# Performance work log

Measured on AMD Instinct MI355X. Metric: run time of the kernel, lower is better.

## Reference

```python
import jax, jax.numpy as jnp
import numpy as np

BETA = 0.25  # commitment loss weight (init kwarg)

def setup_inputs() -> dict:
    key = jax.random.key(0)
    k1, k2 = jax.random.split(key)
    z = jax.random.normal(k1, (4, 256, 16, 32, 32), dtype=jnp.float32)
    # nn.Embedding init: uniform(-1/K, 1/K)
    K, d = 1024, 256
    emb_w = jax.random.uniform(k2, (K, d), dtype=jnp.float32,
                               minval=-1.0 / K, maxval=1.0 / K)
    return {"z": z, "emb_w": emb_w}


def reference(z, emb_w):
    B, C, D, H, W = z.shape  # C == embedding_dim
    zp = jnp.transpose(z, (0, 2, 3, 4, 1))          # (B, D, H, W, C)
    z_flat = zp.reshape(-1, C)                      # (N, C)
    # squared distances ||z - e||^2 = ||z||^2 + ||e||^2 - 2 z.e
    z_sq = jnp.sum(z_flat * z_flat, axis=1, keepdims=True)      # (N, 1)
    e_sq = jnp.sum(emb_w * emb_w, axis=1)[None, :]              # (1, K)
    dist = z_sq + e_sq - 2.0 * jnp.einsum('nc,kc->nk', z_flat, emb_w)  # (N, K)
    idx = jnp.argmin(dist, axis=1)                  # (N,)
    z_q = emb_w[idx]                                # (N, C)
    sg = jax.lax.stop_gradient
    loss = jnp.mean((sg(z_q) - z_flat) ** 2) + BETA * jnp.mean((z_q - sg(z_flat)) ** 2)
    # straight-through estimator
    z_q = z_flat + sg(z_q - z_flat)
    z_q = z_q.reshape(B, D, H, W, C)
    z_q = jnp.transpose(z_q, (0, 4, 1, 2, 3))       # (B, C, D, H, W)
    return z_q, loss, idx
```

## Files before the change

kernel.cpp:

```cpp
#include <hip/hip_runtime.h>

#define KCODES 1024
#define CDIM   256
#define SP     16384
#define ZQTOT  16777216
#define NQ     65536
#define BSTRIDE 4194304
#define MAX_AMB 12288
#define LOSS_SCALE 33554432.0
#define KEYMASK 0xFFFFFC00u
#define AMB_THR 6.0e-4f
#define BIAS    0.25f

#define QT2    128
#define NTILE  32
#define ROWB   528
#define TILEB  16896

using f32x4  = __attribute__((ext_vector_type(4)))  float;
using f32x16 = __attribute__((ext_vector_type(16))) float;
using bf16x8 = __attribute__((ext_vector_type(8)))  short;

__device__ __forceinline__ unsigned short f2bf(float x) {
    unsigned u = __float_as_uint(x);
    u += 0x7fffu + ((u >> 16) & 1u);
    return (unsigned short)(u >> 16);
}
__device__ __forceinline__ unsigned umn(unsigned a, unsigned b){ return a < b ? a : b; }
__device__ __forceinline__ unsigned umx(unsigned a, unsigned b){ return a > b ? a : b; }

__device__ __forceinline__ float pw128_sq(const float* a) {
    float r[8];
    #pragma unroll
    for (int j = 0; j < 8; ++j) r[j] = __fmul_rn(a[j], a[j]);
    for (int i = 8; i < 128; i += 8) {
        #pragma unroll
        for (int j = 0; j < 8; ++j) r[j] = __fadd_rn(r[j], __fmul_rn(a[i+j], a[i+j]));
    }
    return __fadd_rn(__fadd_rn(__fadd_rn(r[0], r[1]), __fadd_rn(r[2], r[3])),
                     __fadd_rn(__fadd_rn(r[4], r[5]), __fadd_rn(r[6], r[7])));
}
__device__ __forceinline__ float pairwise256_sq(const float* a) {
    return __fadd_rn(pw128_sq(a), pw128_sq(a + 128));
}
__device__ __forceinline__ float np_dot256(const float* zr, const float* er) {
    float a0 = 0.f, a1 = 0.f, a2 = 0.f, a3 = 0.f;
    for (int i8 = 0; i8 < 256; i8 += 8) {
        a0 = __fadd_rn(a0, __fmul_rn(zr[i8+0], er[i8+0]));
        a1 = __fadd_rn(a1, __fmul_rn(zr[i8+1], er[i8+1]));
        a2 = __fadd_rn(a2, __fmul_rn(zr[i8+2], er[i8+2]));
        a3 = __fadd_rn(a3, __fmul_rn(zr[i8+3], er[i8+3]));
        a0 = __fadd_rn(a0, __fmul_rn(zr[i8+4], er[i8+4]));
        a1 = __fadd_rn(a1, __fmul_rn(zr[i8+5], er[i8+5]));
        a2 = __fadd_rn(a2, __fmul_rn(zr[i8+6], er[i8+6]));
        a3 = __fadd_rn(a3, __fmul_rn(zr[i8+7], er[i8+7]));
    }
    return __fadd_rn(__fadd_rn(a0, a1), __fadd_rn(a2, a3));
}

__global__ __launch_bounds__(64)
void vq_prep(const float* __restrict__ emb, unsigned short* __restrict__ embh,
             float* __restrict__ esq_g) {
    const int k = blockIdx.x;
    const int l = threadIdx.x;
    float4 v = ((const float4*)(emb + (size_t)k * CDIM))[l];
    float s = v.x*v.x + v.y*v.y + v.z*v.z + v.w*v.w;
    unsigned short h0=f2bf(v.x), h1=f2bf(v.y), h2=f2bf(v.z), h3=f2bf(v.w);
    uint2 hh; hh.x = (unsigned)h0 | ((unsigned)h1<<16); hh.y = (unsigned)h2 | ((unsigned)h3<<16);
    *(uint2*)&embh[(size_t)k*CDIM + l*4] = hh;
    #pragma unroll
    for (int off = 32; off > 0; off >>= 1) s += __shfl_down(s, off, 64);
    if (l == 0) esq_g[k] = s + BIAS;
}

__global__ __launch_bounds__(256, 2)
void vq_main_mfma(const float* __restrict__ z, const float* __restrict__ emb,
                  const unsigned short* __restrict__ embh,
                  const float* __restrict__ esq_g,
                  float* __restrict__ out, unsigned long long* __restrict__ loss_acc,
                  unsigned int* __restrict__ amb_cnt, uint4* __restrict__ wl4) {
    __shared__ __align__(16) unsigned char smem[2*TILEB + 4096];
    unsigned* top1 = (unsigned*)(smem + 2*TILEB);
    unsigned* top2 = top1 + 128;
    unsigned* top3 = top2 + 128;
    float*    zsql = (float*)(top3 + 128);
    int*      fidx = (int*)(zsql + 128);
    float*    lpart = (float*)(fidx + 128);

    const int t    = threadIdx.x;
    const int l    = t & 63;
    const int w    = t >> 6;
    const int half = l >> 5;
    const int lr   = l & 31;
    const int bid  = blockIdx.x;
    const int obid = ((bid & 7) << 6) + (bid >> 3);
    const int n0   = obid * QT2;
    const int b    = n0 >> 14;
    const int sp0  = n0 & 16383;
    const int wq0  = w * 32;
    const float* zb = z + (size_t)b * BSTRIDE + sp0 + wq0 + lr;
    const char* ebase = (const char*)embh;

    uint4 st[4];
    #pragma unroll
    for (int k = 0; k < 4; ++k)
        st[k] = *(const uint4*)(ebase + (size_t)(t + k*256) * 16);

    bf16x8 A[16];
    float zsq_p = 0.f;
    #pragma unroll
    for (int ks = 0; ks < 16; ++ks) {
        const float* zp = zb + (size_t)(ks*16 + half*8) * SP;
        float v[8];
        #pragma unroll
        for (int j = 0; j < 8; ++j) v[j] = zp[(size_t)j * SP];
        bf16x8 a;
        #pragma unroll
        for (int j = 0; j < 8; ++j) {
            zsq_p += v[j] * v[j];
            a[j] = (short)f2bf(v[j]);
        }
        A[ks] = a;
    }
    zsq_p += __shfl_xor(zsq_p, 32, 64);
    if (half == 0) zsql[wq0 + lr] = zsq_p;

    #pragma unroll
    for (int k = 0; k < 4; ++k) {
        const int idx = t + k*256;
        *(uint4*)(smem + (idx >> 5)*ROWB + (idx & 31)*16) = st[k];
    }
    __syncthreads();

    unsigned m1v[16], m2v[16], m3v[16];
    #pragma unroll
    for (int s = 0; s < 16; ++s) { m1v[s]=0xFFFFFFFFu; m2v[s]=0xFFFFFFFFu; m3v[s]=0xFFFFFFFFu; }

    int cur = 0;
    for (int tile = 0; tile < NTILE; ++tile) {
        if (tile + 1 < NTILE) {
            #pragma unroll
            for (int k = 0; k < 4; ++k)
                st[k] = *(const uint4*)(ebase + (size_t)(tile+1)*16384 + (size_t)(t + k*256)*16);
        }
        const float es = esq_g[tile*32 + lr];

        const unsigned char* bb = smem + cur*TILEB + lr*ROWB + half*16;
        f32x16 acc[4];
        #pragma unroll
        for (int c = 0; c < 4; ++c)
            acc[c] = f32x16{0.f,0.f,0.f,0.f,0.f,0.f,0.f,0.f,0.f,0.f,0.f,0.f,0.f,0.f,0.f,0.f};
        __builtin_amdgcn_s_setprio(1);
        #pragma unroll
        for (int ks = 0; ks < 16; ++ks) {
            const bf16x8 Bv = *(const bf16x8*)(bb + ks*32);
            acc[ks & 3] = __builtin_amdgcn_mfma_f32_32x32x16_bf16(A[ks], Bv, acc[ks & 3], 0, 0, 0);
        }
        __builtin_amdgcn_s_setprio(0);
        const unsigned kc = (unsigned)(tile*32 + lr);
        #pragma unroll
        for (int s = 0; s < 16; ++s) {
            const float dot = (acc[0][s] + acc[1][s]) + (acc[2][s] + acc[3][s]);
            const float sc = __builtin_fmaf(-2.0f, dot, es);
            const unsigned p = (__float_as_uint(sc) & KEYMASK) | kc;
            const unsigned x = umx(m1v[s], p); m1v[s] = umn(m1v[s], p);
            const unsigned y = umx(m2v[s], x); m2v[s] = umn(m2v[s], x);
            m3v[s] = umn(m3v[s], y);
        }
        if (tile + 1 < NTILE) {
            #pragma unroll
            for (int k = 0; k < 4; ++k) {
                const int idx = t + k*256;
                *(uint4*)(smem + (cur^1)*TILEB + (idx >> 5)*ROWB + (idx & 31)*16) = st[k];
            }
        }
        __syncthreads();
        cur ^= 1;
    }

    #pragma unroll
    for (int s = 0; s < 16; ++s) {
        unsigned a1 = m1v[s], a2 = m2v[s], a3 = m3v[s];
        #pragma unroll
        for (int m = 1; m < 32; m <<= 1) {
            const unsigned b1 = (unsigned)__shfl_xor((int)a1, m, 64);
            const unsigned b2 = (unsigned)__shfl_xor((int)a2, m, 64);
            const unsigned b3 = (unsigned)__shfl_xor((int)a3, m, 64);
            const unsigned hi1 = umx(a1, b1), lo2 = umn(a2, b2);
            const unsigned r3  = umn(umx(hi1, lo2), umn(a3, b3));
            a1 = umn(a1, b1);
            a2 = umn(hi1, lo2);
            a3 = r3;
        }
        if (lr == s) {
            const int r = (s & 3) + ((s >> 2) << 3) + (half << 2);
            top1[wq0 + r] = a1; top2[wq0 + r] = a2; top3[wq0 + r] = a3;
        }
    }
    __syncthreads();

    if (t < QT2) {
        const unsigned k1 = top1[t], k2 = top2[t], k3 = top3[t];
        const int I1 = (int)(k1 & 1023u);
        fidx[t] = I1;
        out[ZQTOT + 1 + n0 + t] = (float)I1;
        const float v1 = __uint_as_float(k1 & KEYMASK);
        const float v2 = __uint_as_float(k2 & KEYMASK);
        if (v2 - v1 < AMB_THR) {
            unsigned pos = atomicAdd(amb_cnt, 1u);
            if (pos < MAX_AMB)
                wl4[pos] = make_uint4((unsigned)(n0 + t),
                                      (k1 & 1023u) | ((k2 & 1023u) << 16),
                                      (k3 & 1023u) | ((k3 & 1023u) << 16), 0u);
        }
        float lq = zsql[t] + (v1 - BIAS);
        #pragma unroll
        for (int off = 32; off > 0; off >>= 1) lq += __shfl_down(lq, off, 64);
        if ((t & 63) == 0) lpart[t >> 6] = lq;
    }
    __syncthreads();
    if (t == 0)
        atomicAdd(loss_acc, (unsigned long long)(long long)((double)(lpart[0] + lpart[1]) * LOSS_SCALE));

    {
        const int q  = t & 127;
        const int dh = t >> 7;
        const int fq = fidx[q];
        const float4* ev = (const float4*)(emb + (size_t)fq * CDIM + dh * 128);
        float* ob = out + (size_t)b * BSTRIDE + (size_t)dh * 128 * SP + sp0 + q;
        #pragma unroll
        for (int i = 0; i < 32; ++i) {
            const float4 v = ev[i];
            float* o = ob + (size_t)(i * 4) * SP;
            o[0]            = v.x;
            o[SP]           = v.y;
            o[2*SP]         = v.z;
            o[(size_t)3*SP] = v.w;
        }
    }
}

__global__ __launch_bounds__(256)
void vq_fix_cand(const float* __restrict__ z, const float* __restrict__ emb,
                 float* __restrict__ out, const unsigned int* __restrict__ amb_cnt,
                 const uint4* __restrict__ wl4,
                 const unsigned long long* __restrict__ loss_acc) {
    __shared__ float zrow[4][CDIM];
    __shared__ float erow[4][4][CDIM];
    __shared__ float dsh[4][4], esh[4][4];
    __shared__ float zss[4];

    if (blockIdx.x == 0 && threadIdx.x == 0) {
        double mse = (double)(long long)(*loss_acc) / LOSS_SCALE / (double)ZQTOT;
        out[ZQTOT] = (float)(mse * 1.25);
    }

    unsigned cnt = *amb_cnt; if (cnt > MAX_AMB) cnt = MAX_AMB;
    const int t  = threadIdx.x;
    const int wv = t >> 6;
    const int l  = t & 63;
    const unsigned stride = gridDim.x * 4;
    const unsigned nIter = (cnt + stride - 1) / stride;

    for (unsigned j = 0; j < nIter; ++j) {
        __syncthreads();
        const unsigned widx = (unsigned)blockIdx.x * 4 + wv + j * stride;
        const bool active = widx < cnt;
        int n = 0, b = 0, sp = 0;
        int codes[4] = {0, 0, 0, 0};
        if (active) {
            const uint4 e = wl4[widx];
            n = (int)e.x; b = n >> 14; sp = n & 16383;
            codes[0] = (int)(e.y & 1023u); codes[1] = (int)((e.y >> 16) & 1023u);
            codes[2] = (int)(e.z & 1023u); codes[3] = (int)((e.z >> 16) & 1023u);
            #pragma unroll
            for (int i = 0; i < 4; ++i) {
                const int c = l + 64*i;
                zrow[wv][c] = z[(size_t)b * BSTRIDE + (size_t)c * SP + sp];
            }
            const int r = l >> 4, c0 = (l & 15) * 16;
            const float4* src = (const float4*)(emb + (size_t)codes[r] * CDIM + c0);
            float4* dst = (float4*)&erow[wv][r][c0];
            #pragma unroll
            for (int i = 0; i < 4; ++i) dst[i] = src[i];
        }
        __syncthreads();
        if (active) {
            const int role = l >> 4, rr = (l >> 2) & 3, a = l & 3;
            if (role == 0) {
                const float* er = erow[wv][rr];
                const float* zr = zrow[wv];
                float acc = __fmul_rn(zr[a], er[a]);
                for (int i = 1; i < 64; ++i)
                    acc = __fadd_rn(acc, __fmul_rn(zr[4*i + a], er[4*i + a]));
                const float u = __fadd_rn(acc, __shfl_xor(acc, 1, 64));
                const float d = __fadd_rn(u,   __shfl_xor(u,   2, 64));
                if (a == 0) dsh[wv][rr] = d;
            } else if (role == 1 || (role == 2 && rr == 0)) {
                const float* src = (role == 1) ? erow[wv][rr] : zrow[wv];
                float pA = __fmul_rn(src[a],       src[a]);
                float pB = __fmul_rn(src[a+4],     src[a+4]);
                float qA = __fmul_rn(src[128+a],   src[128+a]);
                float qB = __fmul_rn(src[128+a+4], src[128+a+4]);
                #pragma unroll 4
                for (int i = 1; i < 16; ++i) {
                    pA = __fadd_rn(pA, __fmul_rn(src[8*i+a],       src[8*i+a]));
                    pB = __fadd_rn(pB, __fmul_rn(src[8*i+a+4],     src[8*i+a+4]));
                    qA = __fadd_rn(qA, __fmul_rn(src[128+8*i+a],   src[128+8*i+a]));
                    qB = __fadd_rn(qB, __fmul_rn(src[128+8*i+a+4], src[128+8*i+a+4]));
                }
                float uA = __fadd_rn(pA, __shfl_xor(pA, 1, 64));
                float vA = __fadd_rn(uA, __shfl_xor(uA, 2, 64));
                float uB = __fadd_rn(pB, __shfl_xor(pB, 1, 64));
                float vB = __fadd_rn(uB, __shfl_xor(uB, 2, 64));
                const float h0 = __fadd_rn(vA, vB);
                float uC = __fadd_rn(qA, __shfl_xor(qA, 1, 64));
                float vC = __fadd_rn(uC, __shfl_xor(uC, 2, 64));
                float uD = __fadd_rn(qB, __shfl_xor(qB, 1, 64));
                float vD = __fadd_rn(uD, __shfl_xor(uD, 2, 64));
                const float h1 = __fadd_rn(vC, vD);
                const float stot = __fadd_rn(h0, h1);
                if (a == 0) { if (role == 1) esh[wv][rr] = stot; else zss[wv] = stot; }
            }
        }
        __syncthreads();
        if (active && l == 0) {
            float bd = 3.4e38f; int bk = KCODES;
            #pragma unroll
            for (int i = 0; i < 4; ++i) {
                const float d = __fsub_rn(__fadd_rn(zss[wv], esh[wv][i]),
                                          __fmul_rn(2.0f, dsh[wv][i]));
                if (d < bd || (d == bd && codes[i] < bk)) { bd = d; bk = codes[i]; }
            }
            out[ZQTOT + 1 + n] = (float)bk;
        }
    }
}

__global__ __launch_bounds__(256)
void vq_main_basic(const float* __restrict__ z, const float* __restrict__ emb,
                   float* __restrict__ out, unsigned long long* __restrict__ loss_acc,
                   unsigned int* __restrict__ amb_cnt, unsigned int* __restrict__ wl) {
    __shared__ float zlz[64 * CDIM];
    __shared__ float esq[KCODES];
    __shared__ float m1s[4][64], m2s[4][64];
    __shared__ int   i1s[4][64];
    __shared__ int   fidx[64];
    __shared__ float lsum[4];

    const int t  = threadIdx.x;
    const int q  = t & 63;
    const int w  = __builtin_amdgcn_readfirstlane(t >> 6);
    const int qs = q & 7;
    const int n0 = blockIdx.x * 64;
    const int b  = n0 >> 14;
    const int sp0 = n0 & 16383;
    const float* zb = z + (size_t)b * BSTRIDE;

    #pragma unroll 4
    for (int i = 0; i < 64; ++i) {
        int c = (t >> 6) * 64 + i;
        float v = zb[(size_t)c * SP + sp0 + q];
        zlz[q * CDIM + ((((c >> 2) ^ qs) << 2) | (c & 3))] = v;
    }
    for (int k = t; k < KCODES; k += 256) {
        const float4* er = (const float4*)(emb + (size_t)k * CDIM);
        float s = 0.f;
        for (int c4 = 0; c4 < 64; ++c4) {
            float4 e = er[c4];
            s += e.x*e.x + e.y*e.y + e.z*e.z + e.w*e.w;
        }
        esq[k] = s;
    }
    __syncthreads();

    float m1 = 3.4e38f, m2 = 3.4e38f; int i1 = 0;
    const float* zrow = zlz + q * CDIM;
    const int kbase = w * 256;
    for (int kk = 0; kk < 256; kk += 8) {
        const int k0 = kbase + kk;
        float acc[8] = {0,0,0,0,0,0,0,0};
        for (int c4 = 0; c4 < 64; ++c4) {
            float4 zv = *(const float4*)(zrow + ((c4 ^ qs) << 2));
            #pragma unroll
            for (int j = 0; j < 8; ++j) {
                float4 ev = *(const float4*)(emb + (size_t)(k0 + j) * CDIM + (c4 << 2));
                acc[j] += zv.x*ev.x + zv.y*ev.y + zv.z*ev.z + zv.w*ev.w;
            }
        }
        #pragma unroll
        for (int j = 0; j < 8; ++j) {
            float s = esq[k0 + j] - 2.0f * acc[j];
            if (s < m1)      { m2 = m1; m1 = s; i1 = k0 + j; }
            else if (s < m2) { m2 = s; }
        }
    }
    m1s[w][q] = m1; m2s[w][q] = m2; i1s[w][q] = i1;
    __syncthreads();

    if (t < 64) {
        float M1 = 3.4e38f, M2 = 3.4e38f; int I1 = 0;
        for (int g = 0; g < 4; ++g) {
            float v1 = m1s[g][t], v2 = m2s[g][t];
            int   a1 = i1s[g][t];
            if (v1 < M1) { M2 = M1; M1 = v1; I1 = a1; }
            else if (v1 < M2) { M2 = v1; }
            if (v2 < M2) { M2 = v2; }
        }
        if (M2 - M1 < 1.5e-4f) {
            unsigned pos = atomicAdd(amb_cnt, 1u);
            if (pos < MAX_AMB) wl[pos] = n0 + t;
        }
        fidx[t] = I1;
        out[ZQTOT + 1 + n0 + t] = (float)I1;
    }
    __syncthreads();

    const int fq = fidx[q];
    const float* eq = emb + (size_t)fq * CDIM;
    float ls = 0.f;
    #pragma unroll 4
    for (int i = 0; i < 64; ++i) {
        int c = (t >> 6) * 64 + i;
        float zv = zrow[((((c >> 2) ^ qs) << 2) | (c & 3))];
        float ev = eq[c];
        float d = ev - zv;
        ls += d * d;
        out[(size_t)b * BSTRIDE + (size_t)c * SP + sp0 + q] = zv + d;
    }
    #pragma unroll
    for (int off = 32; off > 0; off >>= 1) ls += __shfl_down(ls, off, 64);
    if (q == 0) lsum[w] = ls;
    __syncthreads();
    if (t == 0) {
        float tot = lsum[0] + lsum[1] + lsum[2] + lsum[3];
        atomicAdd(loss_acc, (unsigned long long)(long long)((double)tot * LOSS_SCALE));
    }
}

__global__ __launch_bounds__(256)
void vq_fix_np(const float* __restrict__ z, const float* __restrict__ emb,
               float* __restrict__ out, const unsigned int* __restrict__ amb_cnt,
               const unsigned int* __restrict__ wl) {
    __shared__ float zrow[CDIM];
    __shared__ float zsq_sh;
    __shared__ float rd[256];
    __shared__ int   rk[256];

    unsigned cnt = *amb_cnt; if (cnt > MAX_AMB) cnt = MAX_AMB;
    if (blockIdx.x >= cnt) return;
    const int n = (int)wl[blockIdx.x];
    const int b = n >> 14, sp = n & 16383;
    const int t = threadIdx.x;

    zrow[t] = z[(size_t)b * BSTRIDE + (size_t)t * SP + sp];
    __syncthreads();
    if (t == 0) zsq_sh = pairwise256_sq(zrow);
    __syncthreads();
    const float zsq = zsq_sh;

    float bestd = 3.4e38f; int bestk = KCODES;
    for (int j = 0; j < 4; ++j) {
        const int k = t + 256 * j;
        const float* er = emb + (size_t)k * CDIM;
        const float dot = np_dot256(zrow, er);
        const float es  = pairwise256_sq(er);
        const float d   = __fsub_rn(__fadd_rn(zsq, es), __fmul_rn(2.0f, dot));
        if (d < bestd || (d == bestd && k < bestk)) { bestd = d; bestk = k; }
    }
    rd[t] = bestd; rk[t] = bestk;
    __syncthreads();
    for (int s = 128; s > 0; s >>= 1) {
        if (t < s) {
            float od = rd[t + s]; int ok = rk[t + s];
            if (od < rd[t] || (od == rd[t] && ok < rk[t])) { rd[t] = od; rk[t] = ok; }
        }
        __syncthreads();
    }
    if (t == 0) out[ZQTOT + 1 + n] = (float)rk[0];
}

__global__ void vq_final(const unsigned long long* __restrict__ acc, float* __restrict__ out) {
    if (threadIdx.x == 0 && blockIdx.x == 0) {
        double mse = (double)(long long)acc[0] / LOSS_SCALE / (double)ZQTOT;
        out[ZQTOT] = (float)(mse * 1.25);
    }
}

extern "C" void kernel_launch(void* const* d_in, const int* in_sizes, int n_in,
                              void* d_out, int out_size, void* d_ws, size_t ws_size,
                              hipStream_t stream) {
    const float* z   = (const float*)d_in[0];
    const float* emb = (const float*)d_in[1];
    float* out = (float*)d_out;

    unsigned long long* loss_acc = (unsigned long long*)d_ws;
    unsigned int* amb_cnt = (unsigned int*)((char*)d_ws + 8);
    const size_t WL4_OFF  = 64;
    const size_t ESQ_OFF  = (WL4_OFF + (size_t)MAX_AMB * 16 + 255) & ~(size_t)255;
    const size_t EMBH_OFF = (ESQ_OFF + (size_t)KCODES * 4 + 255) & ~(size_t)255;
    const size_t WS_NEED  = EMBH_OFF + (size_t)KCODES * CDIM * 2;

    hipMemsetAsync(d_ws, 0, 16, stream);
    if (ws_size >= WS_NEED) {
        uint4* wl4 = (uint4*)((char*)d_ws + WL4_OFF);
        float* esq_g = (float*)((char*)d_ws + ESQ_OFF);
        unsigned short* embh = (unsigned short*)((char*)d_ws + EMBH_OFF);
        vq_prep<<<dim3(KCODES), dim3(64), 0, stream>>>(emb, embh, esq_g);
        vq_main_mfma<<<dim3(NQ / QT2), dim3(256), 0, stream>>>(z, emb, embh, esq_g,
                                                               out, loss_acc, amb_cnt, wl4);
        vq_fix_cand<<<dim3(1024), dim3(256), 0, stream>>>(z, emb, out, amb_cnt, wl4, loss_acc);
    } else {
        unsigned int* wl = (unsigned int*)((char*)d_ws + WL4_OFF);
        vq_main_basic<<<dim3(NQ / 64), dim3(256), 0, stream>>>(z, emb, out, loss_acc, amb_cnt, wl);
        vq_fix_np<<<dim3(MAX_AMB), dim3(256), 0, stream>>>(z, emb, out, amb_cnt, wl);
        vq_final<<<dim3(1), dim3(64), 0, stream>>>(loss_acc, out);
    }
}
```

Baseline: 112.6 us.

## Switch main VQ kernel to 16x16x32 MFMA with 64-query blocks

Moves the distance kernel from 32x32x16 MFMA tiles over 128 queries per block to 16x16x32 MFMA tiles over 64 queries per block, with two code sub-tiles per step. Register use for A fragments and per-query top-k state drops, and launch bounds are raised to 4 blocks per SM for higher occupancy. The cross-lane reduction now merges 4 candidates per lane and keeps a true fourth candidate for the ambiguity worklist, instead of repeating the third. In exchange, each block re-streams the full codebook for half as many queries, doubling LDS and L2 traffic per query.

```diff
diff --git a/kernel.cpp b/kernel.cpp
--- a/kernel.cpp
+++ b/kernel.cpp
@@ -12,13 +12,12 @@
 #define AMB_THR 6.0e-4f
 #define BIAS    0.25f
 
-#define QT2    128
+#define QT     64
 #define NTILE  32
 #define ROWB   528
 #define TILEB  16896
 
 using f32x4  = __attribute__((ext_vector_type(4)))  float;
-using f32x16 = __attribute__((ext_vector_type(16))) float;
 using bf16x8 = __attribute__((ext_vector_type(8)))  short;
 
 __device__ __forceinline__ unsigned short f2bf(float x) {
@@ -73,31 +72,31 @@
     if (l == 0) esq_g[k] = s + BIAS;
 }
 
-__global__ __launch_bounds__(256, 2)
+__global__ __launch_bounds__(256, 4)
 void vq_main_mfma(const float* __restrict__ z, const float* __restrict__ emb,
                   const unsigned short* __restrict__ embh,
                   const float* __restrict__ esq_g,
                   float* __restrict__ out, unsigned long long* __restrict__ loss_acc,
                   unsigned int* __restrict__ amb_cnt, uint4* __restrict__ wl4) {
-    __shared__ __align__(16) unsigned char smem[2*TILEB + 4096];
+    __shared__ __align__(16) unsigned char smem[2*TILEB + 2048];
     unsigned* top1 = (unsigned*)(smem + 2*TILEB);
-    unsigned* top2 = top1 + 128;
-    unsigned* top3 = top2 + 128;
-    float*    zsql = (float*)(top3 + 128);
-    int*      fidx = (int*)(zsql + 128);
-    float*    lpart = (float*)(fidx + 128);
-
-    const int t    = threadIdx.x;
-    const int l    = t & 63;
-    const int w    = t >> 6;
-    const int half = l >> 5;
-    const int lr   = l & 31;
+    unsigned* top2 = top1 + 64;
+    unsigned* top3 = top2 + 64;
+    unsigned* top4 = top3 + 64;
+    float*    zsql = (float*)(top4 + 64);
+    int*      fidx = (int*)(zsql + 64);
+
+    const int t  = threadIdx.x;
+    const int l  = t & 63;
+    const int w  = t >> 6;
+    const int lh = l >> 4;
+    const int lr = l & 15;
     const int bid  = blockIdx.x;
-    const int obid = ((bid & 7) << 6) + (bid >> 3);
-    const int n0   = obid * QT2;
+    const int obid = ((bid & 7) << 7) + (bid >> 3);
+    const int n0   = obid * QT;
     const int b    = n0 >> 14;
     const int sp0  = n0 & 16383;
-    const int wq0  = w * 32;
+    const int wq0  = w * 16;
     const float* zb = z + (size_t)b * BSTRIDE + sp0 + wq0 + lr;
     const char* ebase = (const char*)embh;
 
@@ -106,11 +105,11 @@
     for (int k = 0; k < 4; ++k)
         st[k] = *(const uint4*)(ebase + (size_t)(t + k*256) * 16);
 
-    bf16x8 A[16];
+    bf16x8 A[8];
     float zsq_p = 0.f;
     #pragma unroll
-    for (int ks = 0; ks < 16; ++ks) {
-        const float* zp = zb + (size_t)(ks*16 + half*8) * SP;
+    for (int ks = 0; ks < 8; ++ks) {
+        const float* zp = zb + (size_t)(ks*32 + lh*8) * SP;
         float v[8];
         #pragma unroll
         for (int j = 0; j < 8; ++j) v[j] = zp[(size_t)j * SP];
@@ -122,8 +121,9 @@
         }
         A[ks] = a;
     }
+    zsq_p += __shfl_xor(zsq_p, 16, 64);
     zsq_p += __shfl_xor(zsq_p, 32, 64);
-    if (half == 0) zsql[wq0 + lr] = zsq_p;
+    if (lh == 0) zsql[wq0 + lr] = zsq_p;
 
     #pragma unroll
     for (int k = 0; k < 4; ++k) {
@@ -132,9 +132,9 @@
     }
     __syncthreads();
 
-    unsigned m1v[16], m2v[16], m3v[16];
-    #pragma unroll
-    for (int s = 0; s < 16; ++s) { m1v[s]=0xFFFFFFFFu; m2v[s]=0xFFFFFFFFu; m3v[s]=0xFFFFFFFFu; }
+    unsigned m1v[4], m2v[4], m3v[4];
+    #pragma unroll
+    for (int s = 0; s < 4; ++s) { m1v[s]=0xFFFFFFFFu; m2v[s]=0xFFFFFFFFu; m3v[s]=0xFFFFFFFFu; }
 
     int cur = 0;
     for (int tile = 0; tile < NTILE; ++tile) {
@@ -143,29 +143,37 @@
             for (int k = 0; k < 4; ++k)
                 st[k] = *(const uint4*)(ebase + (size_t)(tile+1)*16384 + (size_t)(t + k*256)*16);
         }
-        const float es = esq_g[tile*32 + lr];
-
-        const unsigned char* bb = smem + cur*TILEB + lr*ROWB + half*16;
-        f32x16 acc[4];
-        #pragma unroll
-        for (int c = 0; c < 4; ++c)
-            acc[c] = f32x16{0.f,0.f,0.f,0.f,0.f,0.f,0.f,0.f,0.f,0.f,0.f,0.f,0.f,0.f,0.f,0.f};
+        const float es0 = esq_g[tile*32 + lr];
+        const float es1 = esq_g[tile*32 + 16 + lr];
+
+        const unsigned char* bb = smem + cur*TILEB + lr*ROWB + lh*16;
+        f32x4 acc[2][2];
+        #pragma unroll
+        for (int nt = 0; nt < 2; ++nt)
+            #pragma unroll
+            for (int c = 0; c < 2; ++c) acc[nt][c] = f32x4{0.f,0.f,0.f,0.f};
         __builtin_amdgcn_s_setprio(1);
         #pragma unroll
-        for (int ks = 0; ks < 16; ++ks) {
-            const bf16x8 Bv = *(const bf16x8*)(bb + ks*32);
-            acc[ks & 3] = __builtin_amdgcn_mfma_f32_32x32x16_bf16(A[ks], Bv, acc[ks & 3], 0, 0, 0);
+        for (int ks = 0; ks < 8; ++ks) {
+            const bf16x8 B0 = *(const bf16x8*)(bb + ks*64);
+            const bf16x8 B1 = *(const bf16x8*)(bb + 16*ROWB + ks*64);
+            acc[0][ks & 1] = __builtin_amdgcn_mfma_f32_16x16x32_bf16(A[ks], B0, acc[0][ks & 1], 0, 0, 0);
+            acc[1][ks & 1] = __builtin_amdgcn_mfma_f32_16x16x32_bf16(A[ks], B1, acc[1][ks & 1], 0, 0, 0);
         }
         __builtin_amdgcn_s_setprio(0);
-        const unsigned kc = (unsigned)(tile*32 + lr);
-        #pragma unroll
-        for (int s = 0; s < 16; ++s) {
-            const float dot = (acc[0][s] + acc[1][s]) + (acc[2][s] + acc[3][s]);
-            const float sc = __builtin_fmaf(-2.0f, dot, es);
-            const unsigned p = (__float_as_uint(sc) & KEYMASK) | kc;
-            const unsigned x = umx(m1v[s], p); m1v[s] = umn(m1v[s], p);
-            const unsigned y = umx(m2v[s], x); m2v[s] = umn(m2v[s], x);
-            m3v[s] = umn(m3v[s], y);
+        #pragma unroll
+        for (int nt = 0; nt < 2; ++nt) {
+            const unsigned kc = (unsigned)(tile*32 + nt*16 + lr);
+            const float es = nt ? es1 : es0;
+            #pragma unroll
+            for (int j = 0; j < 4; ++j) {
+                const float dot = acc[nt][0][j] + acc[nt][1][j];
+                const float sc = __builtin_fmaf(-2.0f, dot, es);
+                const unsigned p = (__float_as_uint(sc) & KEYMASK) | kc;
+                const unsigned x = umx(m1v[j], p); m1v[j] = umn(m1v[j], p);
+                const unsigned y = umx(m2v[j], x); m2v[j] = umn(m2v[j], x);
+                m3v[j] = umn(m3v[j], y);
+            }
         }
         if (tile + 1 < NTILE) {
             #pragma unroll
@@ -179,28 +187,30 @@
     }
 
     #pragma unroll
-    for (int s = 0; s < 16; ++s) {
-        unsigned a1 = m1v[s], a2 = m2v[s], a3 = m3v[s];
-        #pragma unroll
-        for (int m = 1; m < 32; m <<= 1) {
-            const unsigned b1 = (unsigned)__shfl_xor((int)a1, m, 64);
-            const unsigned b2 = (unsigned)__shfl_xor((int)a2, m, 64);
-            const unsigned b3 = (unsigned)__shfl_xor((int)a3, m, 64);
-            const unsigned hi1 = umx(a1, b1), lo2 = umn(a2, b2);
-            const unsigned r3  = umn(umx(hi1, lo2), umn(a3, b3));
-            a1 = umn(a1, b1);
-            a2 = umn(hi1, lo2);
-            a3 = r3;
-        }
-        if (lr == s) {
-            const int r = (s & 3) + ((s >> 2) << 3) + (half << 2);
-            top1[wq0 + r] = a1; top2[wq0 + r] = a2; top3[wq0 + r] = a3;
-        }
-    }
-    __syncthreads();
-
-    if (t < QT2) {
-        const unsigned k1 = top1[t], k2 = top2[t], k3 = top3[t];
+    for (int s = 0; s < 4; ++s) {
+        unsigned t1 = m1v[s], t2 = m2v[s], t3 = m3v[s], t4 = 0xFFFFFFFFu;
+        #pragma unroll
+        for (int m = 1; m < 16; m <<= 1) {
+            const unsigned b1 = (unsigned)__shfl_xor((int)t1, m, 64);
+            const unsigned b2 = (unsigned)__shfl_xor((int)t2, m, 64);
+            const unsigned b3 = (unsigned)__shfl_xor((int)t3, m, 64);
+            const unsigned b4 = (unsigned)__shfl_xor((int)t4, m, 64);
+            #define INS(v) { unsigned x_=umx(t1,(v)); t1=umn(t1,(v)); \
+                             unsigned y_=umx(t2,x_);  t2=umn(t2,x_);  \
+                             unsigned z_=umx(t3,y_);  t3=umn(t3,y_);  \
+                             t4=umn(t4,z_); }
+            INS(b1); INS(b2); INS(b3); INS(b4);
+            #undef INS
+        }
+        if (lr == 0) {
+            const int qq = wq0 + lh*4 + s;
+            top1[qq] = t1; top2[qq] = t2; top3[qq] = t3; top4[qq] = t4;
+        }
+    }
+    __syncthreads();
+
+    if (t < QT) {
+        const unsigned k1 = top1[t], k2 = top2[t], k3 = top3[t], k4 = top4[t];
         const int I1 = (int)(k1 & 1023u);
         fidx[t] = I1;
         out[ZQTOT + 1 + n0 + t] = (float)I1;
@@ -211,25 +221,24 @@
             if (pos < MAX_AMB)
                 wl4[pos] = make_uint4((unsigned)(n0 + t),
                                       (k1 & 1023u) | ((k2 & 1023u) << 16),
-                                      (k3 & 1023u) | ((k3 & 1023u) << 16), 0u);
+                                      (k3 & 1023u) | ((k4 & 1023u) << 16), 0u);
         }
         float lq = zsql[t] + (v1 - BIAS);
         #pragma unroll
         for (int off = 32; off > 0; off >>= 1) lq += __shfl_down(lq, off, 64);
-        if ((t & 63) == 0) lpart[t >> 6] = lq;
-    }
-    __syncthreads();
-    if (t == 0)
-        atomicAdd(loss_acc, (unsigned long long)(long long)((double)(lpart[0] + lpart[1]) * LOSS_SCALE));
+        if (t == 0)
+            atomicAdd(loss_acc, (unsigned long long)(long long)((double)lq * LOSS_SCALE));
+    }
+    __syncthreads();
 
     {
-        const int q  = t & 127;
-        const int dh = t >> 7;
+        const int q  = t & 63;
+        const int dh = t >> 6;
         const int fq = fidx[q];
-        const float4* ev = (const float4*)(emb + (size_t)fq * CDIM + dh * 128);
-        float* ob = out + (size_t)b * BSTRIDE + (size_t)dh * 128 * SP + sp0 + q;
-        #pragma unroll
-        for (int i = 0; i < 32; ++i) {
+        const float4* ev = (const float4*)(emb + (size_t)fq * CDIM + dh * 64);
+        float* ob = out + (size_t)b * BSTRIDE + (size_t)dh * 64 * SP + sp0 + q;
+        #pragma unroll
+        for (int i = 0; i < 16; ++i) {
             const float4 v = ev[i];
             float* o = ob + (size_t)(i * 4) * SP;
             o[0]            = v.x;
@@ -507,8 +516,8 @@
         float* esq_g = (float*)((char*)d_ws + ESQ_OFF);
         unsigned short* embh = (unsigned short*)((char*)d_ws + EMBH_OFF);
         vq_prep<<<dim3(KCODES), dim3(64), 0, stream>>>(emb, embh, esq_g);
-        vq_main_mfma<<<dim3(NQ / QT2), dim3(256), 0, stream>>>(z, emb, embh, esq_g,
-                                                               out, loss_acc, amb_cnt, wl4);
+        vq_main_mfma<<<dim3(NQ / QT), dim3(256), 0, stream>>>(z, emb, embh, esq_g,
+                                                              out, loss_acc, amb_cnt, wl4);
         vq_fix_cand<<<dim3(1024), dim3(256), 0, stream>>>(z, emb, out, amb_cnt, wl4, loss_acc);
     } else {
         unsigned int* wl = (unsigned int*)((char*)d_ws + WL4_OFF);
```

Result: no change. 113.5 us (+0.8%).

## Fuse ambiguous-candidate fixup and loss finalization into main MFMA kernel

Applied to the files above, without the earlier changes.

Each block now keeps its ambiguous queries in a shared-memory worklist and rechecks them in exact fp32 at the end of the main kernel, so the separate vq_fix_cand launch and its global worklist and atomics go away. The final loss is written by the last block to finish, detected with a done counter and a threadfence. This saves a kernel launch and global round-trips. In exchange, the per-block worklist is capped at 64 entries, which could drop fixes when a block has many near-ties, and shared memory is reused for the fixup buffers.

```diff
diff --git a/kernel.cpp b/kernel.cpp
--- a/kernel.cpp
+++ b/kernel.cpp
@@ -16,6 +16,7 @@
 #define NTILE  32
 #define ROWB   528
 #define TILEB  16896
+#define WLMAX  64
 
 using f32x4  = __attribute__((ext_vector_type(4)))  float;
 using f32x16 = __attribute__((ext_vector_type(16))) float;
@@ -78,7 +79,7 @@
                   const unsigned short* __restrict__ embh,
                   const float* __restrict__ esq_g,
                   float* __restrict__ out, unsigned long long* __restrict__ loss_acc,
-                  unsigned int* __restrict__ amb_cnt, uint4* __restrict__ wl4) {
+                  unsigned int* __restrict__ done_cnt) {
     __shared__ __align__(16) unsigned char smem[2*TILEB + 4096];
     unsigned* top1 = (unsigned*)(smem + 2*TILEB);
     unsigned* top2 = top1 + 128;
@@ -86,6 +87,13 @@
     float*    zsql = (float*)(top3 + 128);
     int*      fidx = (int*)(zsql + 128);
     float*    lpart = (float*)(fidx + 128);
+    unsigned* wlcnt = (unsigned*)(smem + 2*TILEB + 2576);
+    uint4*    wlloc = (uint4*)(smem + 2*TILEB + 2592);
+    float* zrow = (float*)smem;
+    float* erow = (float*)(smem + 4096);
+    float* dsh  = (float*)(smem + 20480);
+    float* esh  = (float*)(smem + 20544);
+    float* zss  = (float*)(smem + 20608);
 
     const int t    = threadIdx.x;
     const int l    = t & 63;
@@ -101,6 +109,8 @@
     const float* zb = z + (size_t)b * BSTRIDE + sp0 + wq0 + lr;
     const char* ebase = (const char*)embh;
 
+    if (t == 0) *wlcnt = 0;
+
     uint4 st[4];
     #pragma unroll
     for (int k = 0; k < 4; ++k)
@@ -207,11 +217,9 @@
         const float v1 = __uint_as_float(k1 & KEYMASK);
         const float v2 = __uint_as_float(k2 & KEYMASK);
         if (v2 - v1 < AMB_THR) {
-            unsigned pos = atomicAdd(amb_cnt, 1u);
-            if (pos < MAX_AMB)
-                wl4[pos] = make_uint4((unsigned)(n0 + t),
-                                      (k1 & 1023u) | ((k2 & 1023u) << 16),
-                                      (k3 & 1023u) | ((k3 & 1023u) << 16), 0u);
+            const unsigned pos = atomicAdd(wlcnt, 1u);
+            if (pos < WLMAX)
+                wlloc[pos] = make_uint4((unsigned)t, k1 & 1023u, k2 & 1023u, k3 & 1023u);
         }
         float lq = zsql[t] + (v1 - BIAS);
         #pragma unroll
@@ -219,8 +227,17 @@
         if ((t & 63) == 0) lpart[t >> 6] = lq;
     }
     __syncthreads();
-    if (t == 0)
-        atomicAdd(loss_acc, (unsigned long long)(long long)((double)(lpart[0] + lpart[1]) * LOSS_SCALE));
+    if (t == 0) {
+        atomicAdd(loss_acc,
+                  (unsigned long long)(long long)((double)(lpart[0] + lpart[1]) * LOSS_SCALE));
+        __threadfence();
+        const unsigned fin = atomicAdd(done_cnt, 1u);
+        if (fin == (unsigned)gridDim.x - 1u) {
+            const unsigned long long tot = atomicAdd(loss_acc, 0ull);
+            const double mse = (double)(long long)tot / LOSS_SCALE / (double)ZQTOT;
+            out[ZQTOT] = (float)(mse * 1.25);
+        }
+    }
 
     {
         const int q  = t & 127;
@@ -238,49 +255,30 @@
             o[(size_t)3*SP] = v.w;
         }
     }
-}
-
-__global__ __launch_bounds__(256)
-void vq_fix_cand(const float* __restrict__ z, const float* __restrict__ emb,
-                 float* __restrict__ out, const unsigned int* __restrict__ amb_cnt,
-                 const uint4* __restrict__ wl4,
-                 const unsigned long long* __restrict__ loss_acc) {
-    __shared__ float zrow[4][CDIM];
-    __shared__ float erow[4][4][CDIM];
-    __shared__ float dsh[4][4], esh[4][4];
-    __shared__ float zss[4];
-
-    if (blockIdx.x == 0 && threadIdx.x == 0) {
-        double mse = (double)(long long)(*loss_acc) / LOSS_SCALE / (double)ZQTOT;
-        out[ZQTOT] = (float)(mse * 1.25);
-    }
-
-    unsigned cnt = *amb_cnt; if (cnt > MAX_AMB) cnt = MAX_AMB;
-    const int t  = threadIdx.x;
-    const int wv = t >> 6;
-    const int l  = t & 63;
-    const unsigned stride = gridDim.x * 4;
-    const unsigned nIter = (cnt + stride - 1) / stride;
-
+
+    __syncthreads();
+    unsigned cnt = *wlcnt; if (cnt > WLMAX) cnt = WLMAX;
+    const unsigned nIter = (cnt + 3) >> 2;
     for (unsigned j = 0; j < nIter; ++j) {
         __syncthreads();
-        const unsigned widx = (unsigned)blockIdx.x * 4 + wv + j * stride;
+        const unsigned widx = j*4 + (unsigned)w;
         const bool active = widx < cnt;
-        int n = 0, b = 0, sp = 0;
+        int qq = 0;
         int codes[4] = {0, 0, 0, 0};
         if (active) {
-            const uint4 e = wl4[widx];
-            n = (int)e.x; b = n >> 14; sp = n & 16383;
-            codes[0] = (int)(e.y & 1023u); codes[1] = (int)((e.y >> 16) & 1023u);
-            codes[2] = (int)(e.z & 1023u); codes[3] = (int)((e.z >> 16) & 1023u);
+            const uint4 e = wlloc[widx];
+            qq = (int)e.x;
+            codes[0] = (int)e.y; codes[1] = (int)e.z;
+            codes[2] = (int)e.w; codes[3] = (int)e.w;
+            const int sp = sp0 + qq;
             #pragma unroll
             for (int i = 0; i < 4; ++i) {
                 const int c = l + 64*i;
-                zrow[wv][c] = z[(size_t)b * BSTRIDE + (size_t)c * SP + sp];
+                zrow[w*256 + c] = z[(size_t)b * BSTRIDE + (size_t)c * SP + sp];
             }
             const int r = l >> 4, c0 = (l & 15) * 16;
             const float4* src = (const float4*)(emb + (size_t)codes[r] * CDIM + c0);
-            float4* dst = (float4*)&erow[wv][r][c0];
+            float4* dst = (float4*)&erow[(w*4 + r)*256 + c0];
             #pragma unroll
             for (int i = 0; i < 4; ++i) dst[i] = src[i];
         }
@@ -288,16 +286,16 @@
         if (active) {
             const int role = l >> 4, rr = (l >> 2) & 3, a = l & 3;
             if (role == 0) {
-                const float* er = erow[wv][rr];
-                const float* zr = zrow[wv];
+                const float* er = &erow[(w*4 + rr)*256];
+                const float* zr = &zrow[w*256];
                 float acc = __fmul_rn(zr[a], er[a]);
                 for (int i = 1; i < 64; ++i)
                     acc = __fadd_rn(acc, __fmul_rn(zr[4*i + a], er[4*i + a]));
                 const float u = __fadd_rn(acc, __shfl_xor(acc, 1, 64));
                 const float d = __fadd_rn(u,   __shfl_xor(u,   2, 64));
-                if (a == 0) dsh[wv][rr] = d;
+                if (a == 0) dsh[w*4 + rr] = d;
             } else if (role == 1 || (role == 2 && rr == 0)) {
-                const float* src = (role == 1) ? erow[wv][rr] : zrow[wv];
+                const float* src = (role == 1) ? &erow[(w*4 + rr)*256] : &zrow[w*256];
                 float pA = __fmul_rn(src[a],       src[a]);
                 float pB = __fmul_rn(src[a+4],     src[a+4]);
                 float qA = __fmul_rn(src[128+a],   src[128+a]);
@@ -320,7 +318,7 @@
                 float vD = __fadd_rn(uD, __shfl_xor(uD, 2, 64));
                 const float h1 = __fadd_rn(vC, vD);
                 const float stot = __fadd_rn(h0, h1);
-                if (a == 0) { if (role == 1) esh[wv][rr] = stot; else zss[wv] = stot; }
+                if (a == 0) { if (role == 1) esh[w*4 + rr] = stot; else zss[w] = stot; }
             }
         }
         __syncthreads();
@@ -328,11 +326,11 @@
             float bd = 3.4e38f; int bk = KCODES;
             #pragma unroll
             for (int i = 0; i < 4; ++i) {
-                const float d = __fsub_rn(__fadd_rn(zss[wv], esh[wv][i]),
-                                          __fmul_rn(2.0f, dsh[wv][i]));
+                const float d = __fsub_rn(__fadd_rn(zss[w], esh[w*4 + i]),
+                                          __fmul_rn(2.0f, dsh[w*4 + i]));
                 if (d < bd || (d == bd && codes[i] < bk)) { bd = d; bk = codes[i]; }
             }
-            out[ZQTOT + 1 + n] = (float)bk;
+            out[ZQTOT + 1 + n0 + qq] = (float)bk;
         }
     }
 }
@@ -495,7 +493,7 @@
     float* out = (float*)d_out;
 
     unsigned long long* loss_acc = (unsigned long long*)d_ws;
-    unsigned int* amb_cnt = (unsigned int*)((char*)d_ws + 8);
+    unsigned int* cnt_ptr = (unsigned int*)((char*)d_ws + 8);
     const size_t WL4_OFF  = 64;
     const size_t ESQ_OFF  = (WL4_OFF + (size_t)MAX_AMB * 16 + 255) & ~(size_t)255;
     const size_t EMBH_OFF = (ESQ_OFF + (size_t)KCODES * 4 + 255) & ~(size_t)255;
@@ -503,17 +501,15 @@
 
     hipMemsetAsync(d_ws, 0, 16, stream);
     if (ws_size >= WS_NEED) {
-        uint4* wl4 = (uint4*)((char*)d_ws + WL4_OFF);
         float* esq_g = (float*)((char*)d_ws + ESQ_OFF);
         unsigned short* embh = (unsigned short*)((char*)d_ws + EMBH_OFF);
         vq_prep<<<dim3(KCODES), dim3(64), 0, stream>>>(emb, embh, esq_g);
         vq_main_mfma<<<dim3(NQ / QT2), dim3(256), 0, stream>>>(z, emb, embh, esq_g,
-                                                               out, loss_acc, amb_cnt, wl4);
-        vq_fix_cand<<<dim3(1024), dim3(256), 0, stream>>>(z, emb, out, amb_cnt, wl4, loss_acc);
+                                                               out, loss_acc, cnt_ptr);
     } else {
         unsigned int* wl = (unsigned int*)((char*)d_ws + WL4_OFF);
-        vq_main_basic<<<dim3(NQ / 64), dim3(256), 0, stream>>>(z, emb, out, loss_acc, amb_cnt, wl);
-        vq_fix_np<<<dim3(MAX_AMB), dim3(256), 0, stream>>>(z, emb, out, amb_cnt, wl);
+        vq_main_basic<<<dim3(NQ / 64), dim3(256), 0, stream>>>(z, emb, out, loss_acc, cnt_ptr, wl);
+        vq_fix_np<<<dim3(MAX_AMB), dim3(256), 0, stream>>>(z, emb, out, cnt_ptr, wl);
         vq_final<<<dim3(1), dim3(64), 0, stream>>>(loss_acc, out);
     }
 }
```

Measured after the change: 119.7 us. 1.06x slower.
